# Performance work log

Measured on AMD Instinct MI355X. Metric: run time of the kernel, lower is better.

Reference implementation:

```python
import jax, jax.numpy as jnp
import numpy as np

EPS = 0.2          # noise scale (init eps)
N_LAYERS = 3
LAYER_CL = 1
USER_NUM = 100000
ITEM_NUM = 50000
NNZ = 1200000
EMB = 64


def setup_inputs() -> dict:
    key = jax.random.key(0)
    k1, k2, k3, k4, k5, k6 = jax.random.split(key, 6)
    N = USER_NUM + ITEM_NUM
    user_emb = jax.random.normal(k1, (USER_NUM, EMB), dtype=jnp.float32)
    item_emb = jax.random.normal(k2, (ITEM_NUM, EMB), dtype=jnp.float32)
    adj_rows = jax.random.randint(k3, (NNZ,), 0, N, dtype=jnp.int32)
    adj_cols = jax.random.randint(k4, (NNZ,), 0, N, dtype=jnp.int32)
    adj_vals = jax.random.uniform(k5, (NNZ,), dtype=jnp.float32)
    noise = jax.random.uniform(k6, (N_LAYERS, N, EMB), dtype=jnp.float32)  # torch.rand_like per layer
    return {"user_emb": user_emb, "item_emb": item_emb, "adj_rows": adj_rows,
            "adj_cols": adj_cols, "adj_vals": adj_vals, "noise": noise}


def _l2_normalize(x):
    # F.normalize(x, dim=-1): x / max(||x||_2, 1e-12)
    n = jnp.sqrt(jnp.sum(x * x, axis=-1, keepdims=True))
    return x / jnp.maximum(n, 1e-12)


def reference(user_emb, item_emb, adj_rows, adj_cols, adj_vals, noise):
    N = user_emb.shape[0] + item_emb.shape[0]
    ego = jnp.concatenate([user_emb, item_emb], axis=0)  # [N, D]
    acc = jnp.zeros_like(ego)
    cl = ego
    for k in range(N_LAYERS):
        # SpMM: ego <- A @ ego (COO via gather + segment_sum)
        gathered = ego[adj_cols] * adj_vals[:, None]          # [nnz, D]
        ego = jax.ops.segment_sum(gathered, adj_rows, num_segments=N)
        # perturbed=True path: signed, l2-normalized uniform noise
        ego = ego + jnp.sign(ego) * _l2_normalize(noise[k]) * EPS
        acc = acc + ego
        if k == LAYER_CL - 1:
            cl = ego
    final = acc / N_LAYERS  # mean over layers (stack+mean fused)
    u = final[:user_emb.shape[0]]
    i = final[user_emb.shape[0]:]
    u_cl = cl[:user_emb.shape[0]]
    i_cl = cl[user_emb.shape[0]:]
    return (u, i, u_cl, i_cl)
```

## Files before the change

### kernel.cpp

```cpp
#include <hip/hip_runtime.h>

#define EPSV 0.2f
#define USER_NUM 100000
#define ITEM_NUM 50000
#define NTOT 150000
#define NNZ_CNT 1200000
#define EMB 64

typedef float v4f __attribute__((ext_vector_type(4)));
typedef int   v2i __attribute__((ext_vector_type(2)));


__global__ void hist_kernel(const int* __restrict__ rows,
                            int* __restrict__ hist,
                            int* __restrict__ ticket) {
    int e = blockIdx.x * blockDim.x + threadIdx.x;
    if (e < NNZ_CNT) ticket[e] = atomicAdd(&hist[rows[e]], 1);
}

__global__ __launch_bounds__(1024) void alloc_kernel(const int* __restrict__ hist,
                                                     int2* __restrict__ rowrange,
                                                     int* __restrict__ cnt) {
    __shared__ int wsum[16];
    __shared__ int sbase;
    int t = threadIdx.x;
    int i = blockIdx.x * 1024 + t;
    int deg = (i < NTOT) ? hist[i] : 0;
    int lane = t & 63;
    int wid = t >> 6;
    int inc = deg;
    #pragma unroll
    for (int off = 1; off < 64; off <<= 1) {
        int x = __shfl_up(inc, off, 64);
        if (lane >= off) inc += x;
    }
    if (lane == 63) wsum[wid] = inc;
    __syncthreads();
    if (t < 16) {
        int v = wsum[t];
        #pragma unroll
        for (int off = 1; off < 16; off <<= 1) {
            int x = __shfl_up(v, off, 64);
            if (t >= off) v += x;
        }
        wsum[t] = v;
        if (t == 15) sbase = atomicAdd(cnt, v);
    }
    __syncthreads();
    int waveoff = (wid > 0) ? wsum[wid - 1] : 0;
    int excl = sbase + waveoff + inc - deg;
    if (i < NTOT) rowrange[i] = make_int2(excl, excl + deg);
}

__global__ void build_kernel(const int* __restrict__ rows,
                             const int* __restrict__ cols,
                             const float* __restrict__ vals,
                             const int2* __restrict__ rowrange,
                             const int* __restrict__ ticket,
                             int2* __restrict__ csr) {
    int e = blockIdx.x * blockDim.x + threadIdx.x;
    if (e >= NNZ_CNT) return;
    int r = rows[e];
    int slot = rowrange[r].x + ticket[e];
    csr[slot] = make_int2(cols[e], __float_as_int(vals[e]));
}

template <bool CONCAT, bool FINAL_MODE>
__global__ void spmm_perturb_kernel(const float* __restrict__ src,
                                    const float* __restrict__ user_emb,
                                    const float* __restrict__ item_emb,
                                    const int2* __restrict__ rowrange,
                                    const int2* __restrict__ csr,
                                    const float* __restrict__ noise_k,
                                    const float* __restrict__ e1,
                                    const float* __restrict__ e2,
                                    float* __restrict__ out) {
    int wid = threadIdx.x >> 6;
    int lane = threadIdx.x & 63;
    int rsub = lane >> 4;
    int q = lane & 15;
    int row = blockIdx.x * 16 + wid * 4 + rsub;
    if (row >= NTOT) return;
    int2 rr = rowrange[row];
    int beg = rr.x, end = rr.y;
    size_t rowoff = (size_t)row * EMB;
    v4f nv = __builtin_nontemporal_load((const v4f*)(noise_k + rowoff) + q);
    v4f a1 = (v4f)(0.f);
    v4f a2 = (v4f)(0.f);
    if constexpr (FINAL_MODE) {
        a1 = __builtin_nontemporal_load((const v4f*)(e1 + rowoff) + q);
        a2 = ((const v4f*)(e2 + rowoff))[q];
    }
    v4f acc = (v4f)(0.f);
    for (int j = beg; j < end; j += 8) {
        int cb[8];
        float vb[8];
        #pragma unroll
        for (int u = 0; u < 8; ++u) {
            int jj = j + u;
            int idx = (jj < end) ? jj : (end - 1);
            v2i ee = __builtin_nontemporal_load((const v2i*)csr + idx);
            cb[u] = ee.x;
            vb[u] = (jj < end) ? __int_as_float(ee.y) : 0.f;
        }
        #pragma unroll
        for (int u = 0; u < 8; ++u) {
            int c = cb[u];
            const float* base;
            if (CONCAT)
                base = (c < USER_NUM) ? (user_emb + (size_t)c * EMB)
                                      : (item_emb + (size_t)(c - USER_NUM) * EMB);
            else
                base = src + (size_t)c * EMB;
            v4f x = ((const v4f*)base)[q];
            acc.x = fmaf(vb[u], x.x, acc.x);
            acc.y = fmaf(vb[u], x.y, acc.y);
            acc.z = fmaf(vb[u], x.z, acc.z);
            acc.w = fmaf(vb[u], x.w, acc.w);
        }
    }
    float s = nv.x * nv.x + nv.y * nv.y + nv.z * nv.z + nv.w * nv.w;
    #pragma unroll
    for (int off = 8; off > 0; off >>= 1) s += __shfl_xor(s, off, 64);
    float scale = EPSV / fmaxf(sqrtf(s), 1e-12f);
    auto pert = [&](float a, float n) {
        float sg = (a > 0.f) ? 1.f : ((a < 0.f) ? -1.f : 0.f);
        return fmaf(sg * scale, n, a);
    };
    v4f y;
    y.x = pert(acc.x, nv.x);
    y.y = pert(acc.y, nv.y);
    y.z = pert(acc.z, nv.z);
    y.w = pert(acc.w, nv.w);
    if constexpr (FINAL_MODE) {
        const float third = 1.f / 3.f;
        v4f f = (a1 + a2 + y) * third;
        __builtin_nontemporal_store(f, (v4f*)(out + rowoff) + q);
    } else {
        ((v4f*)(out + rowoff))[q] = y;
    }
}

extern "C" void kernel_launch(void* const* d_in, const int* in_sizes, int n_in,
                              void* d_out, int out_size, void* d_ws, size_t ws_size,
                              hipStream_t stream) {
    const float* user_emb = (const float*)d_in[0];
    const float* item_emb = (const float*)d_in[1];
    const int*   adj_rows = (const int*)d_in[2];
    const int*   adj_cols = (const int*)d_in[3];
    const float* adj_vals = (const float*)d_in[4];
    const float* noise    = (const float*)d_in[5];

    float* out_final = (float*)d_out;
    float* out_cl    = (float*)d_out + (size_t)NTOT * EMB;

    char* p = (char*)d_ws;
    float* wsA      = (float*)p;  p += (size_t)NTOT * EMB * sizeof(float);
    int2*  rowrange = (int2*)p;   p += (size_t)NTOT * sizeof(int2);
    int2*  csr      = (int2*)p;   p += (size_t)NNZ_CNT * sizeof(int2);
    int*   ticket   = (int*)p;    p += (size_t)NNZ_CNT * sizeof(int);
    int*   hist     = (int*)p;    p += (size_t)NTOT * sizeof(int);
    int*   cnt      = (int*)p;    p += 16 * sizeof(int);

    (void)hipMemsetAsync(hist, 0, ((size_t)NTOT + 16) * sizeof(int), stream);

    hist_kernel<<<(NNZ_CNT + 255) / 256, 256, 0, stream>>>(adj_rows, hist, ticket);
    alloc_kernel<<<(NTOT + 1023) / 1024, 1024, 0, stream>>>(hist, rowrange, cnt);
    build_kernel<<<(NNZ_CNT + 255) / 256, 256, 0, stream>>>(
        adj_rows, adj_cols, adj_vals, rowrange, ticket, csr);

    const int spmm_blocks = (NTOT + 15) / 16;
    const size_t NE = (size_t)NTOT * EMB;

    spmm_perturb_kernel<true, false><<<spmm_blocks, 256, 0, stream>>>(
        nullptr, user_emb, item_emb, rowrange, csr, noise + 0 * NE,
        nullptr, nullptr, out_cl);
    spmm_perturb_kernel<false, false><<<spmm_blocks, 256, 0, stream>>>(
        out_cl, nullptr, nullptr, rowrange, csr, noise + 1 * NE,
        nullptr, nullptr, wsA);
    spmm_perturb_kernel<false, true><<<spmm_blocks, 256, 0, stream>>>(
        wsA, nullptr, nullptr, rowrange, csr, noise + 2 * NE,
        out_cl, wsA, out_final);
}
```

Before: 451.1 us.

## Fuse CSR build phases into one cooperative kernel with grid syncs

Replaces the separate histogram, row-allocation scan and scatter kernels with a single cooperative kernel of 1024 persistent blocks that uses grid-wide syncs between phases. The aim is to remove two kernel launch gaps and their tail effects. In exchange it adds grid-sync cost, uses grid-stride loops with fewer threads in flight, and the scan now runs in 256-thread chunks, which means more atomic base allocations on cnt.

```diff
diff --git a/kernel.cpp b/kernel.cpp
--- a/kernel.cpp
+++ b/kernel.cpp
@@ -1,4 +1,7 @@
 #include <hip/hip_runtime.h>
+#include <hip/hip_cooperative_groups.h>
+
+namespace cg = cooperative_groups;
 
 #define EPSV 0.2f
 #define USER_NUM 100000
@@ -7,62 +10,68 @@
 #define NNZ_CNT 1200000
 #define EMB 64
 
+#define BUILD_BLOCKS 1024
+#define BUILD_THREADS 256
+
 typedef float v4f __attribute__((ext_vector_type(4)));
 typedef int   v2i __attribute__((ext_vector_type(2)));
 
+__global__ __launch_bounds__(BUILD_THREADS) void csr_build_kernel(
+        const int* __restrict__ rows,
+        const int* __restrict__ cols,
+        const float* __restrict__ vals,
+        int* __restrict__ hist,
+        int* __restrict__ ticket,
+        int2* __restrict__ rowrange,
+        int2* __restrict__ csr,
+        int* __restrict__ cnt) {
+    cg::grid_group grid = cg::this_grid();
+    const int t = threadIdx.x;
+    const int gstride = BUILD_BLOCKS * BUILD_THREADS;
 
-__global__ void hist_kernel(const int* __restrict__ rows,
-                            int* __restrict__ hist,
-                            int* __restrict__ ticket) {
-    int e = blockIdx.x * blockDim.x + threadIdx.x;
-    if (e < NNZ_CNT) ticket[e] = atomicAdd(&hist[rows[e]], 1);
-}
+    for (int e = blockIdx.x * BUILD_THREADS + t; e < NNZ_CNT; e += gstride)
+        ticket[e] = atomicAdd(&hist[rows[e]], 1);
 
-__global__ __launch_bounds__(1024) void alloc_kernel(const int* __restrict__ hist,
-                                                     int2* __restrict__ rowrange,
-                                                     int* __restrict__ cnt) {
-    __shared__ int wsum[16];
-    __shared__ int sbase;
-    int t = threadIdx.x;
-    int i = blockIdx.x * 1024 + t;
-    int deg = (i < NTOT) ? hist[i] : 0;
-    int lane = t & 63;
-    int wid = t >> 6;
-    int inc = deg;
-    #pragma unroll
-    for (int off = 1; off < 64; off <<= 1) {
-        int x = __shfl_up(inc, off, 64);
-        if (lane >= off) inc += x;
+    grid.sync();
+
+    {
+        __shared__ int wsum[4];
+        __shared__ int wpre[4];
+        __shared__ int sbase;
+        const int lane = t & 63;
+        const int wid = t >> 6;
+        const int nchunks = (NTOT + BUILD_THREADS - 1) / BUILD_THREADS;
+        for (int chunk = blockIdx.x; chunk < nchunks; chunk += BUILD_BLOCKS) {
+            int i = chunk * BUILD_THREADS + t;
+            int deg = (i < NTOT) ? hist[i] : 0;
+            int inc = deg;
+            #pragma unroll
+            for (int off = 1; off < 64; off <<= 1) {
+                int x = __shfl_up(inc, off, 64);
+                if (lane >= off) inc += x;
+            }
+            if (lane == 63) wsum[wid] = inc;
+            __syncthreads();
+            if (t == 0) {
+                int run = 0;
+                #pragma unroll
+                for (int w = 0; w < 4; ++w) { wpre[w] = run; run += wsum[w]; }
+                sbase = atomicAdd(cnt, run);
+            }
+            __syncthreads();
+            int excl = sbase + wpre[wid] + inc - deg;
+            if (i < NTOT) rowrange[i] = make_int2(excl, excl + deg);
+            __syncthreads();
+        }
     }
-    if (lane == 63) wsum[wid] = inc;
-    __syncthreads();
-    if (t < 16) {
-        int v = wsum[t];
-        #pragma unroll
-        for (int off = 1; off < 16; off <<= 1) {
-            int x = __shfl_up(v, off, 64);
-            if (t >= off) v += x;
-        }
-        wsum[t] = v;
-        if (t == 15) sbase = atomicAdd(cnt, v);
+
+    grid.sync();
+
+    for (int e = blockIdx.x * BUILD_THREADS + t; e < NNZ_CNT; e += gstride) {
+        int r = rows[e];
+        int slot = rowrange[r].x + ticket[e];
+        csr[slot] = make_int2(cols[e], __float_as_int(vals[e]));
     }
-    __syncthreads();
-    int waveoff = (wid > 0) ? wsum[wid - 1] : 0;
-    int excl = sbase + waveoff + inc - deg;
-    if (i < NTOT) rowrange[i] = make_int2(excl, excl + deg);
-}
-
-__global__ void build_kernel(const int* __restrict__ rows,
-                             const int* __restrict__ cols,
-                             const float* __restrict__ vals,
-                             const int2* __restrict__ rowrange,
-                             const int* __restrict__ ticket,
-                             int2* __restrict__ csr) {
-    int e = blockIdx.x * blockDim.x + threadIdx.x;
-    if (e >= NNZ_CNT) return;
-    int r = rows[e];
-    int slot = rowrange[r].x + ticket[e];
-    csr[slot] = make_int2(cols[e], __float_as_int(vals[e]));
 }
 
 template <bool CONCAT, bool FINAL_MODE>
@@ -164,10 +173,14 @@
 
     (void)hipMemsetAsync(hist, 0, ((size_t)NTOT + 16) * sizeof(int), stream);
 
-    hist_kernel<<<(NNZ_CNT + 255) / 256, 256, 0, stream>>>(adj_rows, hist, ticket);
-    alloc_kernel<<<(NTOT + 1023) / 1024, 1024, 0, stream>>>(hist, rowrange, cnt);
-    build_kernel<<<(NNZ_CNT + 255) / 256, 256, 0, stream>>>(
-        adj_rows, adj_cols, adj_vals, rowrange, ticket, csr);
+    {
+        void* args[] = {(void*)&adj_rows, (void*)&adj_cols, (void*)&adj_vals,
+                        (void*)&hist, (void*)&ticket, (void*)&rowrange,
+                        (void*)&csr, (void*)&cnt};
+        (void)hipLaunchCooperativeKernel((void*)csr_build_kernel,
+                                         dim3(BUILD_BLOCKS), dim3(BUILD_THREADS),
+                                         args, 0, stream);
+    }
 
     const int spmm_blocks = (NTOT + 15) / 16;
     const size_t NE = (size_t)NTOT * EMB;
```

Result: slower. 652.3 us (+44.6%).

## Build CSR with per-slice counting and deterministic slice-local scatter offsets

Applied to the files above, without the earlier changes.

Replaces the device-wide atomic histogram and per-edge ticket array with 32 edge slices. Each slice keeps its own row-count array, stored in the scratch embedding buffer. The alloc kernel sums the slice counts, computes the row ranges, and turns each slice count into a start offset. The scatter kernel then places edges using workgroup-scoped atomics. This removes the ticket array and the global-atomic contention, but runs only 32 blocks and adds about 19 MB of count traffic, which may leave most of the GPU idle during CSR build.

```diff
diff --git a/kernel.cpp b/kernel.cpp
--- a/kernel.cpp
+++ b/kernel.cpp
@@ -7,25 +7,38 @@
 #define NNZ_CNT 1200000
 #define EMB 64
 
+#define G_SLICES 32
+#define SLICE_E (NNZ_CNT / G_SLICES)
+
 typedef float v4f __attribute__((ext_vector_type(4)));
 typedef int   v2i __attribute__((ext_vector_type(2)));
 
 
-__global__ void hist_kernel(const int* __restrict__ rows,
-                            int* __restrict__ hist,
-                            int* __restrict__ ticket) {
-    int e = blockIdx.x * blockDim.x + threadIdx.x;
-    if (e < NNZ_CNT) ticket[e] = atomicAdd(&hist[rows[e]], 1);
-}
-
-__global__ __launch_bounds__(1024) void alloc_kernel(const int* __restrict__ hist,
+__global__ __launch_bounds__(1024) void count_kernel(const int* __restrict__ rows,
+                                                     int* __restrict__ count) {
+    const int w = blockIdx.x;
+    const int t = threadIdx.x;
+    int* mine = count + (size_t)w * NTOT;
+    for (int i = t; i < NTOT; i += 1024) mine[i] = 0;
+    __syncthreads();
+    const int e0 = w * SLICE_E;
+    for (int e = e0 + t; e < e0 + SLICE_E; e += 1024)
+        __hip_atomic_fetch_add(&mine[rows[e]], 1, __ATOMIC_RELAXED,
+                               __HIP_MEMORY_SCOPE_WORKGROUP);
+}
+
+__global__ __launch_bounds__(1024) void alloc_kernel(int* __restrict__ count,
                                                      int2* __restrict__ rowrange,
                                                      int* __restrict__ cnt) {
     __shared__ int wsum[16];
     __shared__ int sbase;
     int t = threadIdx.x;
     int i = blockIdx.x * 1024 + t;
-    int deg = (i < NTOT) ? hist[i] : 0;
+    int deg = 0;
+    if (i < NTOT) {
+        #pragma unroll
+        for (int w = 0; w < G_SLICES; ++w) deg += count[(size_t)w * NTOT + i];
+    }
     int lane = t & 63;
     int wid = t >> 6;
     int inc = deg;
@@ -49,20 +62,33 @@
     __syncthreads();
     int waveoff = (wid > 0) ? wsum[wid - 1] : 0;
     int excl = sbase + waveoff + inc - deg;
-    if (i < NTOT) rowrange[i] = make_int2(excl, excl + deg);
-}
-
-__global__ void build_kernel(const int* __restrict__ rows,
-                             const int* __restrict__ cols,
-                             const float* __restrict__ vals,
-                             const int2* __restrict__ rowrange,
-                             const int* __restrict__ ticket,
-                             int2* __restrict__ csr) {
-    int e = blockIdx.x * blockDim.x + threadIdx.x;
-    if (e >= NNZ_CNT) return;
-    int r = rows[e];
-    int slot = rowrange[r].x + ticket[e];
-    csr[slot] = make_int2(cols[e], __float_as_int(vals[e]));
+    if (i < NTOT) {
+        rowrange[i] = make_int2(excl, excl + deg);
+        int run = excl;
+        #pragma unroll
+        for (int w = 0; w < G_SLICES; ++w) {
+            int c = count[(size_t)w * NTOT + i];
+            count[(size_t)w * NTOT + i] = run;
+            run += c;
+        }
+    }
+}
+
+__global__ __launch_bounds__(1024) void scatter_kernel(const int* __restrict__ rows,
+                                                       const int* __restrict__ cols,
+                                                       const float* __restrict__ vals,
+                                                       int* __restrict__ count,
+                                                       int2* __restrict__ csr) {
+    const int w = blockIdx.x;
+    const int t = threadIdx.x;
+    int* cur = count + (size_t)w * NTOT;
+    const int e0 = w * SLICE_E;
+    for (int e = e0 + t; e < e0 + SLICE_E; e += 1024) {
+        int r = rows[e];
+        int slot = __hip_atomic_fetch_add(&cur[r], 1, __ATOMIC_RELAXED,
+                                          __HIP_MEMORY_SCOPE_WORKGROUP);
+        csr[slot] = make_int2(cols[e], __float_as_int(vals[e]));
+    }
 }
 
 template <bool CONCAT, bool FINAL_MODE>
@@ -158,16 +184,16 @@
     float* wsA      = (float*)p;  p += (size_t)NTOT * EMB * sizeof(float);
     int2*  rowrange = (int2*)p;   p += (size_t)NTOT * sizeof(int2);
     int2*  csr      = (int2*)p;   p += (size_t)NNZ_CNT * sizeof(int2);
-    int*   ticket   = (int*)p;    p += (size_t)NNZ_CNT * sizeof(int);
-    int*   hist     = (int*)p;    p += (size_t)NTOT * sizeof(int);
     int*   cnt      = (int*)p;    p += 16 * sizeof(int);
 
-    (void)hipMemsetAsync(hist, 0, ((size_t)NTOT + 16) * sizeof(int), stream);
-
-    hist_kernel<<<(NNZ_CNT + 255) / 256, 256, 0, stream>>>(adj_rows, hist, ticket);
-    alloc_kernel<<<(NTOT + 1023) / 1024, 1024, 0, stream>>>(hist, rowrange, cnt);
-    build_kernel<<<(NNZ_CNT + 255) / 256, 256, 0, stream>>>(
-        adj_rows, adj_cols, adj_vals, rowrange, ticket, csr);
+    int* count = (int*)wsA;
+
+    (void)hipMemsetAsync(cnt, 0, 16 * sizeof(int), stream);
+
+    count_kernel<<<G_SLICES, 1024, 0, stream>>>(adj_rows, count);
+    alloc_kernel<<<(NTOT + 1023) / 1024, 1024, 0, stream>>>(count, rowrange, cnt);
+    scatter_kernel<<<G_SLICES, 1024, 0, stream>>>(adj_rows, adj_cols, adj_vals,
+                                                  count, csr);
 
     const int spmm_blocks = (NTOT + 15) / 16;
     const size_t NE = (size_t)NTOT * EMB;
```

Measured after the change: 655.7 us. 45.3% more time.

## Build CSR via two-level bucket sort with shared-memory atomics

Applied to the files above, without the earlier changes.

Replaces the global-atomic histogram, scan and scatter CSR build with a two-level counting sort. Edges are first bucketed by row>>7 using per-block shared-memory histograms, a column scan and a scatter. Each 128-row bucket is then sorted locally in shared memory, with the local row packed into the high bits of the column index. This removes 1.2M contended global atomics and the memset, and makes the bucket writes more local. The cost is an extra pass over the edges and a scan done by a single block.

```diff
diff --git a/kernel.cpp b/kernel.cpp
--- a/kernel.cpp
+++ b/kernel.cpp
@@ -7,62 +7,134 @@
 #define NNZ_CNT 1200000
 #define EMB 64
 
+#define RPB 128
+#define NBUCK ((NTOT + RPB - 1) / RPB)
+#define BLKA 128
+#define SLICE_E (NNZ_CNT / BLKA)
+
 typedef float v4f __attribute__((ext_vector_type(4)));
 typedef int   v2i __attribute__((ext_vector_type(2)));
 
 
-__global__ void hist_kernel(const int* __restrict__ rows,
-                            int* __restrict__ hist,
-                            int* __restrict__ ticket) {
-    int e = blockIdx.x * blockDim.x + threadIdx.x;
-    if (e < NNZ_CNT) ticket[e] = atomicAdd(&hist[rows[e]], 1);
-}
-
-__global__ __launch_bounds__(1024) void alloc_kernel(const int* __restrict__ hist,
-                                                     int2* __restrict__ rowrange,
-                                                     int* __restrict__ cnt) {
-    __shared__ int wsum[16];
-    __shared__ int sbase;
-    int t = threadIdx.x;
-    int i = blockIdx.x * 1024 + t;
-    int deg = (i < NTOT) ? hist[i] : 0;
-    int lane = t & 63;
-    int wid = t >> 6;
-    int inc = deg;
+__global__ __launch_bounds__(256) void bucket_count_kernel(const int* __restrict__ rows,
+                                                           int* __restrict__ bcount) {
+    __shared__ int lh[NBUCK];
+    const int t = threadIdx.x, blk = blockIdx.x;
+    for (int b = t; b < NBUCK; b += 256) lh[b] = 0;
+    __syncthreads();
+    const int e0 = blk * SLICE_E;
+    for (int e = e0 + t; e < e0 + SLICE_E; e += 256)
+        atomicAdd(&lh[rows[e] >> 7], 1);
+    __syncthreads();
+    int* out = bcount + (size_t)blk * NBUCK;
+    for (int b = t; b < NBUCK; b += 256) out[b] = lh[b];
+}
+
+__global__ __launch_bounds__(1024) void bucket_scan_kernel(int* __restrict__ bcount,
+                                                           int* __restrict__ bucketStart) {
+    __shared__ int tot[NBUCK];
+    __shared__ int wsums[16];
+    const int t = threadIdx.x;
+    for (int b = t; b < NBUCK; b += 1024) {
+        int run = 0;
+        int* col = bcount + b;
+        #pragma unroll 8
+        for (int blk = 0; blk < BLKA; ++blk) {
+            int v = col[(size_t)blk * NBUCK];
+            col[(size_t)blk * NBUCK] = run;
+            run += v;
+        }
+        tot[b] = run;
+    }
+    __syncthreads();
+    int e0 = 2 * t, e1 = 2 * t + 1;
+    int c0 = (e0 < NBUCK) ? tot[e0] : 0;
+    int c1 = (e1 < NBUCK) ? tot[e1] : 0;
+    int v = c0 + c1;
+    int lane = t & 63, wid = t >> 6;
+    int inc = v;
     #pragma unroll
     for (int off = 1; off < 64; off <<= 1) {
         int x = __shfl_up(inc, off, 64);
         if (lane >= off) inc += x;
     }
-    if (lane == 63) wsum[wid] = inc;
+    if (lane == 63) wsums[wid] = inc;
     __syncthreads();
     if (t < 16) {
-        int v = wsum[t];
+        int w = wsums[t];
         #pragma unroll
         for (int off = 1; off < 16; off <<= 1) {
-            int x = __shfl_up(v, off, 64);
-            if (t >= off) v += x;
-        }
-        wsum[t] = v;
-        if (t == 15) sbase = atomicAdd(cnt, v);
-    }
-    __syncthreads();
-    int waveoff = (wid > 0) ? wsum[wid - 1] : 0;
-    int excl = sbase + waveoff + inc - deg;
-    if (i < NTOT) rowrange[i] = make_int2(excl, excl + deg);
-}
-
-__global__ void build_kernel(const int* __restrict__ rows,
-                             const int* __restrict__ cols,
-                             const float* __restrict__ vals,
-                             const int2* __restrict__ rowrange,
-                             const int* __restrict__ ticket,
-                             int2* __restrict__ csr) {
-    int e = blockIdx.x * blockDim.x + threadIdx.x;
-    if (e >= NNZ_CNT) return;
-    int r = rows[e];
-    int slot = rowrange[r].x + ticket[e];
-    csr[slot] = make_int2(cols[e], __float_as_int(vals[e]));
+            int x = __shfl_up(w, off, 64);
+            if (t >= off) w += x;
+        }
+        wsums[t] = w;
+    }
+    __syncthreads();
+    int waveoff = (wid > 0) ? wsums[wid - 1] : 0;
+    int excl = waveoff + inc - v;
+    if (e0 < NBUCK) bucketStart[e0] = excl;
+    if (e1 < NBUCK) bucketStart[e1] = excl + c0;
+    if (t == 0) bucketStart[NBUCK] = NNZ_CNT;
+}
+
+__global__ __launch_bounds__(256) void bucket_scatter_kernel(const int* __restrict__ rows,
+                                                             const int* __restrict__ cols,
+                                                             const float* __restrict__ vals,
+                                                             const int* __restrict__ bcount,
+                                                             const int* __restrict__ bucketStart,
+                                                             int2* __restrict__ ebuf) {
+    __shared__ int cur[NBUCK];
+    const int t = threadIdx.x, blk = blockIdx.x;
+    const int* mine = bcount + (size_t)blk * NBUCK;
+    for (int b = t; b < NBUCK; b += 256) cur[b] = bucketStart[b] + mine[b];
+    __syncthreads();
+    const int e0 = blk * SLICE_E;
+    for (int e = e0 + t; e < e0 + SLICE_E; e += 256) {
+        int r = rows[e];
+        int pos = atomicAdd(&cur[r >> 7], 1);
+        ebuf[pos] = make_int2(cols[e] | ((r & 127) << 20), __float_as_int(vals[e]));
+    }
+}
+
+__global__ __launch_bounds__(256) void bucket_csr_kernel(const int2* __restrict__ ebuf,
+                                                         const int* __restrict__ bucketStart,
+                                                         int2* __restrict__ rowrange,
+                                                         int2* __restrict__ csr) {
+    __shared__ int h[RPB];
+    __shared__ int c[RPB];
+    __shared__ int wst[4];
+    const int t = threadIdx.x, b = blockIdx.x;
+    const int base = bucketStart[b];
+    const int n = bucketStart[b + 1] - base;
+    if (t < RPB) h[t] = 0;
+    __syncthreads();
+    for (int i = t; i < n; i += 256)
+        atomicAdd(&h[(ebuf[base + i].x >> 20) & 127], 1);
+    __syncthreads();
+    int lane = t & 63, wid = t >> 6;
+    int v = (t < RPB) ? h[t] : 0;
+    int inc = v;
+    #pragma unroll
+    for (int off = 1; off < 64; off <<= 1) {
+        int x = __shfl_up(inc, off, 64);
+        if (lane >= off) inc += x;
+    }
+    if (lane == 63) wst[wid] = inc;
+    __syncthreads();
+    int woff = (wid == 1) ? wst[0] : 0;
+    int excl = woff + inc - v;
+    if (t < RPB) {
+        c[t] = excl;
+        int r0 = b * RPB + t;
+        if (r0 < NTOT) rowrange[r0] = make_int2(base + excl, base + excl + v);
+    }
+    __syncthreads();
+    for (int i = t; i < n; i += 256) {
+        int2 cc = ebuf[base + i];
+        int lr = (cc.x >> 20) & 127;
+        int pos = atomicAdd(&c[lr], 1);
+        csr[base + pos] = make_int2(cc.x & 0xFFFFF, cc.y);
+    }
 }
 
 template <bool CONCAT, bool FINAL_MODE>
@@ -158,16 +230,17 @@
     float* wsA      = (float*)p;  p += (size_t)NTOT * EMB * sizeof(float);
     int2*  rowrange = (int2*)p;   p += (size_t)NTOT * sizeof(int2);
     int2*  csr      = (int2*)p;   p += (size_t)NNZ_CNT * sizeof(int2);
-    int*   ticket   = (int*)p;    p += (size_t)NNZ_CNT * sizeof(int);
-    int*   hist     = (int*)p;    p += (size_t)NTOT * sizeof(int);
-    int*   cnt      = (int*)p;    p += 16 * sizeof(int);
-
-    (void)hipMemsetAsync(hist, 0, ((size_t)NTOT + 16) * sizeof(int), stream);
-
-    hist_kernel<<<(NNZ_CNT + 255) / 256, 256, 0, stream>>>(adj_rows, hist, ticket);
-    alloc_kernel<<<(NTOT + 1023) / 1024, 1024, 0, stream>>>(hist, rowrange, cnt);
-    build_kernel<<<(NNZ_CNT + 255) / 256, 256, 0, stream>>>(
-        adj_rows, adj_cols, adj_vals, rowrange, ticket, csr);
+
+    char* q = (char*)wsA;
+    int2* ebuf        = (int2*)q;  q += (size_t)NNZ_CNT * sizeof(int2);
+    int*  bcount      = (int*)q;   q += (size_t)BLKA * NBUCK * sizeof(int);
+    int*  bucketStart = (int*)q;   q += (size_t)(NBUCK + 1) * sizeof(int);
+
+    bucket_count_kernel<<<BLKA, 256, 0, stream>>>(adj_rows, bcount);
+    bucket_scan_kernel<<<1, 1024, 0, stream>>>(bcount, bucketStart);
+    bucket_scatter_kernel<<<BLKA, 256, 0, stream>>>(adj_rows, adj_cols, adj_vals,
+                                                    bcount, bucketStart, ebuf);
+    bucket_csr_kernel<<<NBUCK, 256, 0, stream>>>(ebuf, bucketStart, rowrange, csr);
 
     const int spmm_blocks = (NTOT + 15) / 16;
     const size_t NE = (size_t)NTOT * EMB;
```

After: 452.9 us. About the same (+0.4%).
